# Optimization experiments

Measured on AMD Instinct MI355X. Metric: run time of the kernel, lower is better.

## Reference

```python
import jax, jax.numpy as jnp
import numpy as np

B, L, D = 8, 4096, 256
H, C = 2, 128
DEG = 16  # incoming ring neighbors per node (excluding self loop)


def _build_edge_index():
    # Block-diagonal graph replicated per batch element, like _get_buffer.
    i = np.arange(L)
    offs = np.arange(1, DEG + 1)
    src_g = ((i[:, None] + offs[None, :]) % L).reshape(-1)   # [L*DEG]
    dst_g = np.repeat(i, DEG)                                 # [L*DEG]
    base = (np.arange(B) * L)[:, None]
    src = (src_g[None, :] + base).reshape(-1)
    dst = (dst_g[None, :] + base).reshape(-1)
    # PyG GATConv: remove_self_loops + add_self_loops -> exactly one self loop/node
    self_idx = np.arange(B * L)
    src = np.concatenate([src, self_idx])
    dst = np.concatenate([dst, self_idx])
    return jnp.asarray(np.stack([src, dst]), dtype=jnp.int32)  # [2, E]


def setup_inputs() -> dict:
    key = jax.random.key(0)
    k0, k1, k2, k3 = jax.random.split(key, 4)
    glorot = 1.0 / np.sqrt(D)
    return {
        "x": jax.random.normal(k0, (B, L, D), jnp.float32),
        "edge_index": _build_edge_index(),
        "W": jax.random.normal(k1, (D, H * C), jnp.float32) * glorot,
        "att_src": jax.random.normal(k2, (H, C), jnp.float32) * (1.0 / np.sqrt(C)),
        "att_dst": jax.random.normal(k3, (H, C), jnp.float32) * (1.0 / np.sqrt(C)),
        "bias": jnp.zeros((H * C,), jnp.float32),
    }


def reference(x, edge_index, W, att_src, att_dst, bias):
    b, l, d = x.shape
    n = b * l
    h_, c_ = att_src.shape
    xf = x.reshape(n, d)                                   # flatten batch of graphs
    res = xf
    h = (xf @ W).reshape(n, h_, c_)                        # [N,H,C] projected features
    a_src = jnp.einsum('nhc,hc->nh', h, att_src)           # per-node src logits
    a_dst = jnp.einsum('nhc,hc->nh', h, att_dst)
    s, t = edge_index[0], edge_index[1]
    alpha = jax.nn.leaky_relu(a_src[s] + a_dst[t], 0.2)    # [E,H]
    # softmax over incoming edges of each destination node
    amax = jax.ops.segment_max(alpha, t, num_segments=n)
    ex = jnp.exp(alpha - amax[t])
    denom = jax.ops.segment_sum(ex, t, num_segments=n)
    attn = ex / jnp.where(denom[t] > 0, denom[t], 1.0)     # [E,H]
    msg = h[s] * attn[:, :, None]                          # [E,H,C]
    out = jax.ops.segment_sum(msg, t, num_segments=n).reshape(n, h_ * c_) + bias
    out = jax.nn.relu(out) + res                           # relu + residual
    return out.reshape(b, l, h_ * c_)
```

## Files before the change

### kernel.cpp

```cpp
#include <hip/hip_runtime.h>

#define LL 4096
#define DD 256
#define TM 32
#define HALO 16
#define ROWS (TM + HALO)
#define NTH 256
#define APAD 40
#define HTS 56
#define WBS 40
#define ABUF_BYTES (ROWS * APAD * 2)

typedef float f32x4 __attribute__((ext_vector_type(4)));
typedef __bf16 bf16x8 __attribute__((ext_vector_type(8)));
typedef unsigned short us8 __attribute__((ext_vector_type(8)));
typedef unsigned short us4 __attribute__((ext_vector_type(4)));
typedef unsigned int u32x2 __attribute__((ext_vector_type(2)));

__device__ __forceinline__ unsigned short f2bf(float f) {
    union { float f; unsigned u; } v; v.f = f;
    unsigned r = v.u + 0x7fffu + ((v.u >> 16) & 1u);
    return (unsigned short)(r >> 16);
}

__device__ __forceinline__ unsigned cvtpk_bf16(float a, float b) {
    unsigned r;
    asm("v_cvt_pk_bf16_f32 %0, %1, %2" : "=v"(r) : "v"(a), "v"(b));
    return r;
}

#define KBAR() do {                                         \
    asm volatile("s_waitcnt lgkmcnt(0)" ::: "memory");      \
    __builtin_amdgcn_s_barrier();                           \
} while (0)

__global__ void prep_w(const float* __restrict__ W, unsigned short* __restrict__ Wt) {
    __shared__ unsigned short wl[32][260];
    const int tid = threadIdx.x;
    const int kk = blockIdx.x;
    for (int lin = tid; lin < 2048; lin += 512) {
        int r = lin >> 6;
        int q = lin & 63;
        const float4 v = *reinterpret_cast<const float4*>(W + (kk * 32 + r) * 256 + q * 4);
        us4 p;
        p[0] = f2bf(v.x); p[1] = f2bf(v.y); p[2] = f2bf(v.z); p[3] = f2bf(v.w);
        *reinterpret_cast<us4*>(&wl[r][q * 4]) = p;
    }
    __syncthreads();
    for (int id = tid; id < 1024; id += 512) {
        int ct = id >> 6, l = id & 63;
        int lo = l & 15, hi = l >> 4;
        us8 v;
        for (int j = 0; j < 8; ++j) v[j] = wl[hi * 8 + j][ct * 16 + lo];
        *reinterpret_cast<us8*>(Wt + (size_t)(((ct * 8 + kk) * 64 + l) * 8)) = v;
    }
}

__global__ __launch_bounds__(NTH, 4) void gat_fused(
    const float* __restrict__ x, const unsigned short* __restrict__ Wt,
    const float* __restrict__ att_src, const float* __restrict__ att_dst,
    const float* __restrict__ bias, float* __restrict__ out)
{
    __shared__ unsigned short h_t[256][HTS];
    __shared__ float alog[ROWS][2][2];
    __shared__ __align__(16) unsigned char smem_u[2 * ABUF_BYTES];
    unsigned short (*abuf0)[APAD] = reinterpret_cast<unsigned short(*)[APAD]>(smem_u);
    unsigned short (*abuf1)[APAD] = reinterpret_cast<unsigned short(*)[APAD]>(smem_u + ABUF_BYTES);
    unsigned short (*wband)[WBS]  = reinterpret_cast<unsigned short(*)[WBS]>(smem_u);

    const int tid  = threadIdx.x;
    const int lane = tid & 63;
    const int wv   = tid >> 6;
    const int lo   = lane & 15;
    const int hi   = lane >> 4;
    const int blk  = (blockIdx.x & 7) * 128 + (blockIdx.x >> 3);
    const int batch = blk >> 7;
    const int i0    = (blk & 127) * TM;
    const long xbase = (long)batch * (LL * DD);
    const int ct0 = wv * 4;
    const int hd  = wv >> 1;

    if (tid < 192) ((float*)alog)[tid] = 0.f;

    f32x4 acc[3][4];
    for (int a = 0; a < 3; ++a)
        for (int b = 0; b < 4; ++b)
            acc[a][b] = (f32x4){0.f, 0.f, 0.f, 0.f};

    const int s0r = tid >> 3, s0k = (tid & 7) << 2;
    const int s1r = (tid + 256) >> 3, s1k = (tid & 7) << 2;
    const float* xrow0 = x + xbase + (long)((i0 + s0r) & (LL - 1)) * DD + s0k;
    const float* xrow1 = x + xbase + (long)((i0 + s1r) & (LL - 1)) * DD + s1k;
    const unsigned short* wtb0 = Wt + (size_t)((ct0 + 0) * 8 * 64 + lane) * 8;
    const unsigned short* wtb1 = Wt + (size_t)((ct0 + 1) * 8 * 64 + lane) * 8;
    const unsigned short* wtb2 = Wt + (size_t)((ct0 + 2) * 8 * 64 + lane) * 8;
    const unsigned short* wtb3 = Wt + (size_t)((ct0 + 3) * 8 * 64 + lane) * 8;

    float4 cur0, cur1, nxt0, nxt1;
    us8 braw0, braw1, braw2, braw3;

    cur0 = *reinterpret_cast<const float4*>(xrow0);
    if (tid < 128) cur1 = *reinterpret_cast<const float4*>(xrow1);
    braw0 = *reinterpret_cast<const us8*>(wtb0);
    braw1 = *reinterpret_cast<const us8*>(wtb1);
    braw2 = *reinterpret_cast<const us8*>(wtb2);
    braw3 = *reinterpret_cast<const us8*>(wtb3);
    {
        u32x2 p;
        p[0] = cvtpk_bf16(cur0.x, cur0.y);
        p[1] = cvtpk_bf16(cur0.z, cur0.w);
        *reinterpret_cast<u32x2*>(&abuf0[s0r][s0k]) = p;
        if (tid < 128) {
            u32x2 q;
            q[0] = cvtpk_bf16(cur1.x, cur1.y);
            q[1] = cvtpk_bf16(cur1.z, cur1.w);
            *reinterpret_cast<u32x2*>(&abuf0[s1r][s1k]) = q;
        }
    }

#pragma unroll
    for (int kk = 0; kk < 8; ++kk) {
        unsigned short (*buf)[APAD]  = (kk & 1) ? abuf1 : abuf0;
        unsigned short (*nbuf)[APAD] = (kk & 1) ? abuf0 : abuf1;
        if (kk < 7) {
            nxt0 = *reinterpret_cast<const float4*>(xrow0 + (kk + 1) * 32);
            if (tid < 128) nxt1 = *reinterpret_cast<const float4*>(xrow1 + (kk + 1) * 32);
        }
        KBAR();

        bf16x8 bf0 = __builtin_bit_cast(bf16x8, braw0);
        bf16x8 bf1 = __builtin_bit_cast(bf16x8, braw1);
        bf16x8 bf2 = __builtin_bit_cast(bf16x8, braw2);
        bf16x8 bf3 = __builtin_bit_cast(bf16x8, braw3);
        for (int rt = 0; rt < 3; ++rt) {
            us8 araw = *reinterpret_cast<const us8*>(&buf[rt * 16 + lo][hi * 8]);
            bf16x8 afrag = __builtin_bit_cast(bf16x8, araw);
            acc[rt][0] = __builtin_amdgcn_mfma_f32_16x16x32_bf16(bf0, afrag, acc[rt][0], 0, 0, 0);
            acc[rt][1] = __builtin_amdgcn_mfma_f32_16x16x32_bf16(bf1, afrag, acc[rt][1], 0, 0, 0);
            acc[rt][2] = __builtin_amdgcn_mfma_f32_16x16x32_bf16(bf2, afrag, acc[rt][2], 0, 0, 0);
            acc[rt][3] = __builtin_amdgcn_mfma_f32_16x16x32_bf16(bf3, afrag, acc[rt][3], 0, 0, 0);
        }

        if (kk < 7) {
            braw0 = *reinterpret_cast<const us8*>(wtb0 + (size_t)(kk + 1) * 512);
            braw1 = *reinterpret_cast<const us8*>(wtb1 + (size_t)(kk + 1) * 512);
            braw2 = *reinterpret_cast<const us8*>(wtb2 + (size_t)(kk + 1) * 512);
            braw3 = *reinterpret_cast<const us8*>(wtb3 + (size_t)(kk + 1) * 512);
            u32x2 p;
            p[0] = cvtpk_bf16(nxt0.x, nxt0.y);
            p[1] = cvtpk_bf16(nxt0.z, nxt0.w);
            *reinterpret_cast<u32x2*>(&nbuf[s0r][s0k]) = p;
            if (tid < 128) {
                u32x2 q;
                q[0] = cvtpk_bf16(nxt1.x, nxt1.y);
                q[1] = cvtpk_bf16(nxt1.z, nxt1.w);
                *reinterpret_cast<u32x2*>(&nbuf[s1r][s1k]) = q;
            }
        }
    }

    {
        float4 as[4], ad[4];
#pragma unroll
        for (int c = 0; c < 4; ++c) {
            as[c] = *reinterpret_cast<const float4*>(att_src + (ct0 + c) * 16 + hi * 4);
            ad[c] = *reinterpret_cast<const float4*>(att_dst + (ct0 + c) * 16 + hi * 4);
        }
        float ps[3], pd[3];
        for (int rt = 0; rt < 3; ++rt) {
            ps[rt] = 0.f; pd[rt] = 0.f;
            int xrow = rt * 16 + lo;
#pragma unroll
            for (int c = 0; c < 4; ++c) {
                f32x4 a = acc[rt][c];
                ps[rt] += a[0] * as[c].x + a[1] * as[c].y + a[2] * as[c].z + a[3] * as[c].w;
                pd[rt] += a[0] * ad[c].x + a[1] * ad[c].y + a[2] * ad[c].z + a[3] * ad[c].w;
                unsigned pk0 = cvtpk_bf16(a[0], a[1]);
                unsigned pk1 = cvtpk_bf16(a[2], a[3]);
                int chan = (ct0 + c) * 16 + hi * 4;
                h_t[chan + 0][xrow] = (unsigned short)pk0;
                h_t[chan + 1][xrow] = (unsigned short)(pk0 >> 16);
                h_t[chan + 2][xrow] = (unsigned short)pk1;
                h_t[chan + 3][xrow] = (unsigned short)(pk1 >> 16);
            }
        }
        for (int rt = 0; rt < 3; ++rt) {
            ps[rt] += __shfl_xor(ps[rt], 16);
            ps[rt] += __shfl_xor(ps[rt], 32);
            pd[rt] += __shfl_xor(pd[rt], 16);
            pd[rt] += __shfl_xor(pd[rt], 32);
        }
        if (hi == 0) {
            for (int rt = 0; rt < 3; ++rt) {
                atomicAdd(&alog[rt * 16 + lo][hd][0], ps[rt]);
                atomicAdd(&alog[rt * 16 + lo][hd][1], pd[rt]);
            }
        }
    }

    float4 res[2][4];
    for (int ti = 0; ti < 2; ++ti)
#pragma unroll
        for (int c = 0; c < 4; ++c)
            res[ti][c] = *reinterpret_cast<const float4*>(
                x + xbase + (long)(i0 + ti * 16 + lo) * DD + (ct0 + c) * 16 + hi * 4);

    __syncthreads();

    if (tid < 64) {
        int r = tid >> 1, h2 = tid & 1;
        unsigned short* wrow = &wband[h2 * 32 + r][0];
        us8 z = {0, 0, 0, 0, 0, 0, 0, 0};
        for (int q = 0; q < 5; ++q) *reinterpret_cast<us8*>(wrow + q * 8) = z;
        float ad = alog[r][h2][1];
        float al[17];
        float mx = -1e30f;
        for (int k = 0; k < 17; ++k) {
            float s = (k < 16) ? alog[r + 1 + k][h2][0] : alog[r][h2][0];
            float v = s + ad;
            v = (v > 0.f) ? v : 0.2f * v;
            al[k] = v;
            mx = fmaxf(mx, v);
        }
        float sum = 0.f;
        for (int k = 0; k < 17; ++k) { al[k] = __expf(al[k] - mx); sum += al[k]; }
        float inv = 1.f / sum;
        int lo_r = r & 15;
        wrow[lo_r] = f2bf(al[16] * inv);
        for (int k = 0; k < 16; ++k) wrow[lo_r + 1 + k] = f2bf(al[k] * inv);
    }
    __syncthreads();

    {
        f32x4 acc2[2][4];
        for (int a = 0; a < 2; ++a)
            for (int b = 0; b < 4; ++b)
                acc2[a][b] = (f32x4){0.f, 0.f, 0.f, 0.f};

        for (int ti = 0; ti < 2; ++ti) {
            us8 raw = *reinterpret_cast<const us8*>(&wband[hd * 32 + ti * 16 + lo][hi * 8]);
            bf16x8 bfr = __builtin_bit_cast(bf16x8, raw);
#pragma unroll
            for (int c = 0; c < 4; ++c) {
                us8 araw = *reinterpret_cast<const us8*>(
                    &h_t[(ct0 + c) * 16 + lo][ti * 16 + hi * 8]);
                bf16x8 afr = __builtin_bit_cast(bf16x8, araw);
                acc2[ti][c] = __builtin_amdgcn_mfma_f32_16x16x32_bf16(afr, bfr, acc2[ti][c], 0, 0, 0);
            }
        }

        for (int ti = 0; ti < 2; ++ti)
#pragma unroll
            for (int c = 0; c < 4; ++c) {
                const float4 b4 = *reinterpret_cast<const float4*>(bias + (ct0 + c) * 16 + hi * 4);
                f32x4 s = acc2[ti][c];
                long g = xbase + (long)(i0 + ti * 16 + lo) * DD + (ct0 + c) * 16 + hi * 4;
                float4 o;
                o.x = fmaxf(s[0] + b4.x, 0.f) + res[ti][c].x;
                o.y = fmaxf(s[1] + b4.y, 0.f) + res[ti][c].y;
                o.z = fmaxf(s[2] + b4.z, 0.f) + res[ti][c].z;
                o.w = fmaxf(s[3] + b4.w, 0.f) + res[ti][c].w;
                *reinterpret_cast<float4*>(out + g) = o;
            }
    }
}

extern "C" void kernel_launch(void* const* d_in, const int* in_sizes, int n_in,
                              void* d_out, int out_size, void* d_ws, size_t ws_size,
                              hipStream_t stream) {
    const float* x       = (const float*)d_in[0];
    const float* W       = (const float*)d_in[2];
    const float* att_src = (const float*)d_in[3];
    const float* att_dst = (const float*)d_in[4];
    const float* bias    = (const float*)d_in[5];
    float* out           = (float*)d_out;
    unsigned short* Wt   = (unsigned short*)d_ws;

    hipLaunchKernelGGL(prep_w, dim3(8), dim3(512), 0, stream, W, Wt);
    hipLaunchKernelGGL(gat_fused, dim3(1024), dim3(NTH), 0, stream,
                       x, Wt, att_src, att_dst, bias, out);
}
```

Before: 30.17 us.

## Use single 64-wide K staging buffer with two barriers instead of double buffering

Replaces the double-buffered 32-wide K staging of bf16-converted x rows with a single 64-wide buffer. Each outer step now covers two MFMA K-slices. This halves the number of outer iterations and lets all threads issue uniform loads, with no tid<128 guard. The cost is a second barrier per step, since the single buffer must not be overwritten while it is still being read. That exposes load latency more, because the next x chunk can only be written after all waves finish the current step.

```diff
diff --git a/kernel.cpp b/kernel.cpp
--- a/kernel.cpp
+++ b/kernel.cpp
@@ -6,10 +6,9 @@
 #define HALO 16
 #define ROWS (TM + HALO)
 #define NTH 256
-#define APAD 40
+#define APAD 72
 #define HTS 56
 #define WBS 40
-#define ABUF_BYTES (ROWS * APAD * 2)
 
 typedef float f32x4 __attribute__((ext_vector_type(4)));
 typedef __bf16 bf16x8 __attribute__((ext_vector_type(8)));
@@ -63,9 +62,8 @@
 {
     __shared__ unsigned short h_t[256][HTS];
     __shared__ float alog[ROWS][2][2];
-    __shared__ __align__(16) unsigned char smem_u[2 * ABUF_BYTES];
-    unsigned short (*abuf0)[APAD] = reinterpret_cast<unsigned short(*)[APAD]>(smem_u);
-    unsigned short (*abuf1)[APAD] = reinterpret_cast<unsigned short(*)[APAD]>(smem_u + ABUF_BYTES);
+    __shared__ __align__(16) unsigned char smem_u[ROWS * APAD * 2];
+    unsigned short (*abuf)[APAD]  = reinterpret_cast<unsigned short(*)[APAD]>(smem_u);
     unsigned short (*wband)[WBS]  = reinterpret_cast<unsigned short(*)[WBS]>(smem_u);
 
     const int tid  = threadIdx.x;
@@ -87,75 +85,94 @@
         for (int b = 0; b < 4; ++b)
             acc[a][b] = (f32x4){0.f, 0.f, 0.f, 0.f};
 
-    const int s0r = tid >> 3, s0k = (tid & 7) << 2;
-    const int s1r = (tid + 256) >> 3, s1k = (tid & 7) << 2;
-    const float* xrow0 = x + xbase + (long)((i0 + s0r) & (LL - 1)) * DD + s0k;
-    const float* xrow1 = x + xbase + (long)((i0 + s1r) & (LL - 1)) * DD + s1k;
+    const int srow = tid >> 4;
+    const int scol = (tid & 15) << 2;
+    const float* xp0 = x + xbase + (long)((i0 + srow     ) & (LL - 1)) * DD + scol;
+    const float* xp1 = x + xbase + (long)((i0 + srow + 16) & (LL - 1)) * DD + scol;
+    const float* xp2 = x + xbase + (long)((i0 + srow + 32) & (LL - 1)) * DD + scol;
     const unsigned short* wtb0 = Wt + (size_t)((ct0 + 0) * 8 * 64 + lane) * 8;
     const unsigned short* wtb1 = Wt + (size_t)((ct0 + 1) * 8 * 64 + lane) * 8;
     const unsigned short* wtb2 = Wt + (size_t)((ct0 + 2) * 8 * 64 + lane) * 8;
     const unsigned short* wtb3 = Wt + (size_t)((ct0 + 3) * 8 * 64 + lane) * 8;
 
-    float4 cur0, cur1, nxt0, nxt1;
+    float4 v0, v1, v2;
     us8 braw0, braw1, braw2, braw3;
 
-    cur0 = *reinterpret_cast<const float4*>(xrow0);
-    if (tid < 128) cur1 = *reinterpret_cast<const float4*>(xrow1);
+    v0 = *reinterpret_cast<const float4*>(xp0);
+    v1 = *reinterpret_cast<const float4*>(xp1);
+    v2 = *reinterpret_cast<const float4*>(xp2);
     braw0 = *reinterpret_cast<const us8*>(wtb0);
     braw1 = *reinterpret_cast<const us8*>(wtb1);
     braw2 = *reinterpret_cast<const us8*>(wtb2);
     braw3 = *reinterpret_cast<const us8*>(wtb3);
     {
         u32x2 p;
-        p[0] = cvtpk_bf16(cur0.x, cur0.y);
-        p[1] = cvtpk_bf16(cur0.z, cur0.w);
-        *reinterpret_cast<u32x2*>(&abuf0[s0r][s0k]) = p;
-        if (tid < 128) {
-            u32x2 q;
-            q[0] = cvtpk_bf16(cur1.x, cur1.y);
-            q[1] = cvtpk_bf16(cur1.z, cur1.w);
-            *reinterpret_cast<u32x2*>(&abuf0[s1r][s1k]) = q;
-        }
-    }
-
-#pragma unroll
-    for (int kk = 0; kk < 8; ++kk) {
-        unsigned short (*buf)[APAD]  = (kk & 1) ? abuf1 : abuf0;
-        unsigned short (*nbuf)[APAD] = (kk & 1) ? abuf0 : abuf1;
-        if (kk < 7) {
-            nxt0 = *reinterpret_cast<const float4*>(xrow0 + (kk + 1) * 32);
-            if (tid < 128) nxt1 = *reinterpret_cast<const float4*>(xrow1 + (kk + 1) * 32);
+        p[0] = cvtpk_bf16(v0.x, v0.y); p[1] = cvtpk_bf16(v0.z, v0.w);
+        *reinterpret_cast<u32x2*>(&abuf[srow][scol]) = p;
+        p[0] = cvtpk_bf16(v1.x, v1.y); p[1] = cvtpk_bf16(v1.z, v1.w);
+        *reinterpret_cast<u32x2*>(&abuf[srow + 16][scol]) = p;
+        p[0] = cvtpk_bf16(v2.x, v2.y); p[1] = cvtpk_bf16(v2.z, v2.w);
+        *reinterpret_cast<u32x2*>(&abuf[srow + 32][scol]) = p;
+    }
+
+#pragma unroll
+    for (int kk = 0; kk < 4; ++kk) {
+        if (kk < 3) {
+            v0 = *reinterpret_cast<const float4*>(xp0 + (kk + 1) * 64);
+            v1 = *reinterpret_cast<const float4*>(xp1 + (kk + 1) * 64);
+            v2 = *reinterpret_cast<const float4*>(xp2 + (kk + 1) * 64);
         }
         KBAR();
 
-        bf16x8 bf0 = __builtin_bit_cast(bf16x8, braw0);
-        bf16x8 bf1 = __builtin_bit_cast(bf16x8, braw1);
-        bf16x8 bf2 = __builtin_bit_cast(bf16x8, braw2);
-        bf16x8 bf3 = __builtin_bit_cast(bf16x8, braw3);
-        for (int rt = 0; rt < 3; ++rt) {
-            us8 araw = *reinterpret_cast<const us8*>(&buf[rt * 16 + lo][hi * 8]);
-            bf16x8 afrag = __builtin_bit_cast(bf16x8, araw);
-            acc[rt][0] = __builtin_amdgcn_mfma_f32_16x16x32_bf16(bf0, afrag, acc[rt][0], 0, 0, 0);
-            acc[rt][1] = __builtin_amdgcn_mfma_f32_16x16x32_bf16(bf1, afrag, acc[rt][1], 0, 0, 0);
-            acc[rt][2] = __builtin_amdgcn_mfma_f32_16x16x32_bf16(bf2, afrag, acc[rt][2], 0, 0, 0);
-            acc[rt][3] = __builtin_amdgcn_mfma_f32_16x16x32_bf16(bf3, afrag, acc[rt][3], 0, 0, 0);
-        }
-
-        if (kk < 7) {
-            braw0 = *reinterpret_cast<const us8*>(wtb0 + (size_t)(kk + 1) * 512);
-            braw1 = *reinterpret_cast<const us8*>(wtb1 + (size_t)(kk + 1) * 512);
-            braw2 = *reinterpret_cast<const us8*>(wtb2 + (size_t)(kk + 1) * 512);
-            braw3 = *reinterpret_cast<const us8*>(wtb3 + (size_t)(kk + 1) * 512);
+        {
+            bf16x8 bf0 = __builtin_bit_cast(bf16x8, braw0);
+            bf16x8 bf1 = __builtin_bit_cast(bf16x8, braw1);
+            bf16x8 bf2 = __builtin_bit_cast(bf16x8, braw2);
+            bf16x8 bf3 = __builtin_bit_cast(bf16x8, braw3);
+            for (int rt = 0; rt < 3; ++rt) {
+                us8 araw = *reinterpret_cast<const us8*>(&abuf[rt * 16 + lo][hi * 8]);
+                bf16x8 afrag = __builtin_bit_cast(bf16x8, araw);
+                acc[rt][0] = __builtin_amdgcn_mfma_f32_16x16x32_bf16(bf0, afrag, acc[rt][0], 0, 0, 0);
+                acc[rt][1] = __builtin_amdgcn_mfma_f32_16x16x32_bf16(bf1, afrag, acc[rt][1], 0, 0, 0);
+                acc[rt][2] = __builtin_amdgcn_mfma_f32_16x16x32_bf16(bf2, afrag, acc[rt][2], 0, 0, 0);
+                acc[rt][3] = __builtin_amdgcn_mfma_f32_16x16x32_bf16(bf3, afrag, acc[rt][3], 0, 0, 0);
+            }
+            braw0 = *reinterpret_cast<const us8*>(wtb0 + (size_t)(2 * kk + 1) * 512);
+            braw1 = *reinterpret_cast<const us8*>(wtb1 + (size_t)(2 * kk + 1) * 512);
+            braw2 = *reinterpret_cast<const us8*>(wtb2 + (size_t)(2 * kk + 1) * 512);
+            braw3 = *reinterpret_cast<const us8*>(wtb3 + (size_t)(2 * kk + 1) * 512);
+        }
+        {
+            bf16x8 bf0 = __builtin_bit_cast(bf16x8, braw0);
+            bf16x8 bf1 = __builtin_bit_cast(bf16x8, braw1);
+            bf16x8 bf2 = __builtin_bit_cast(bf16x8, braw2);
+            bf16x8 bf3 = __builtin_bit_cast(bf16x8, braw3);
+            for (int rt = 0; rt < 3; ++rt) {
+                us8 araw = *reinterpret_cast<const us8*>(&abuf[rt * 16 + lo][32 + hi * 8]);
+                bf16x8 afrag = __builtin_bit_cast(bf16x8, araw);
+                acc[rt][0] = __builtin_amdgcn_mfma_f32_16x16x32_bf16(bf0, afrag, acc[rt][0], 0, 0, 0);
+                acc[rt][1] = __builtin_amdgcn_mfma_f32_16x16x32_bf16(bf1, afrag, acc[rt][1], 0, 0, 0);
+                acc[rt][2] = __builtin_amdgcn_mfma_f32_16x16x32_bf16(bf2, afrag, acc[rt][2], 0, 0, 0);
+                acc[rt][3] = __builtin_amdgcn_mfma_f32_16x16x32_bf16(bf3, afrag, acc[rt][3], 0, 0, 0);
+            }
+            if (kk < 3) {
+                braw0 = *reinterpret_cast<const us8*>(wtb0 + (size_t)(2 * kk + 2) * 512);
+                braw1 = *reinterpret_cast<const us8*>(wtb1 + (size_t)(2 * kk + 2) * 512);
+                braw2 = *reinterpret_cast<const us8*>(wtb2 + (size_t)(2 * kk + 2) * 512);
+                braw3 = *reinterpret_cast<const us8*>(wtb3 + (size_t)(2 * kk + 2) * 512);
+            }
+        }
+
+        KBAR();
+
+        if (kk < 3) {
             u32x2 p;
-            p[0] = cvtpk_bf16(nxt0.x, nxt0.y);
-            p[1] = cvtpk_bf16(nxt0.z, nxt0.w);
-            *reinterpret_cast<u32x2*>(&nbuf[s0r][s0k]) = p;
-            if (tid < 128) {
-                u32x2 q;
-                q[0] = cvtpk_bf16(nxt1.x, nxt1.y);
-                q[1] = cvtpk_bf16(nxt1.z, nxt1.w);
-                *reinterpret_cast<u32x2*>(&nbuf[s1r][s1k]) = q;
-            }
+            p[0] = cvtpk_bf16(v0.x, v0.y); p[1] = cvtpk_bf16(v0.z, v0.w);
+            *reinterpret_cast<u32x2*>(&abuf[srow][scol]) = p;
+            p[0] = cvtpk_bf16(v1.x, v1.y); p[1] = cvtpk_bf16(v1.z, v1.w);
+            *reinterpret_cast<u32x2*>(&abuf[srow + 16][scol]) = p;
+            p[0] = cvtpk_bf16(v2.x, v2.y); p[1] = cvtpk_bf16(v2.z, v2.w);
+            *reinterpret_cast<u32x2*>(&abuf[srow + 32][scol]) = p;
         }
     }
 
```

Result: no change. 30.45 us (+0.9%).
